# Performance work log

Hardware: AMD Instinct MI355X
Metric: run time of the kernel (lower is better)

Reference implementation:

```python
import jax, jax.numpy as jnp
import numpy as np
from jax import lax

DIM = 1152
HEADS = 16
HEAD_DIM = 72  # HEADS*HEAD_DIM == DIM
HID = 4608     # int(DIM*4.0)
B = 2
N = 4096
EPS_RMS = 1e-6
EPS_LA = 1e-15


def setup_inputs() -> dict:
    key = jax.random.key(0)
    ks = jax.random.split(key, 12)
    w = lambda k, shape: (jax.random.normal(k, shape, jnp.float32) * 0.02)
    z = lambda n: jnp.zeros((n,), jnp.float32)
    return {
        "hidden_states": jax.random.normal(ks[0], (B, N, DIM), jnp.float32),
        "temb": jax.random.normal(ks[1], (B, 6 * DIM), jnp.float32),
        "scale_shift_table": jax.random.normal(ks[2], (6, DIM), jnp.float32) / np.float32(np.sqrt(DIM)),
        "Wq": w(ks[3], (DIM, DIM)), "bq": z(DIM),
        "Wk": w(ks[4], (DIM, DIM)), "bk": z(DIM),
        "Wv": w(ks[5], (DIM, DIM)), "bv": z(DIM),
        "Wo": w(ks[6], (DIM, DIM)), "bo": z(DIM),
        "W_inv": w(ks[7], (2 * HID, DIM)), "b_inv": z(2 * HID),   # 1x1 conv dim -> 2*hid
        "W_dw": w(ks[8], (2 * HID, 3)), "b_dw": z(2 * HID),       # depthwise k=3
        "W_pt": w(ks[9], (DIM, HID)),                              # 1x1 conv hid -> dim, no bias
    }


def _rms(x):
    # RMSNorm, elementwise_affine=False, eps=1e-6
    return x * lax.rsqrt(jnp.mean(x * x, axis=-1, keepdims=True) + EPS_RMS)


def reference(hidden_states, temb, scale_shift_table, Wq, bq, Wk, bk, Wv, bv, Wo, bo,
              W_inv, b_inv, W_dw, b_dw, W_pt):
    Bn, Nn, D = hidden_states.shape
    # adaLN-single modulation
    mods = scale_shift_table[None] + temb.reshape(Bn, 6, D)  # (B,6,D)
    shift_msa, scale_msa, gate_msa, shift_mlp, scale_mlp, gate_mlp = (
        mods[:, i][:, None, :] for i in range(6))  # each (B,1,D)

    x = _rms(hidden_states) * (1.0 + scale_msa) + shift_msa

    # --- Lite linear attention (ReLU kernel, denominator via padded-ones value) ---
    q = jax.nn.relu(x @ Wq.T + bq).reshape(Bn, Nn, HEADS, HEAD_DIM).transpose(0, 2, 1, 3)  # bhnd
    k = jax.nn.relu(x @ Wk.T + bk).reshape(Bn, Nn, HEADS, HEAD_DIM).transpose(0, 2, 1, 3)
    v = (x @ Wv.T + bv).reshape(Bn, Nn, HEADS, HEAD_DIM).transpose(0, 2, 1, 3)
    v = jnp.pad(v, ((0, 0), (0, 0), (0, 0), (0, 1)), constant_values=1.0)  # (B,h,N,d+1)
    kv = jnp.einsum('bhnd,bhne->bhde', k, v)        # (B,h,d,d+1)
    out = jnp.einsum('bhnd,bhde->bhne', q, kv)      # (B,h,N,d+1)
    out = out[..., :-1] / (out[..., -1:] + EPS_LA)  # numerator / denominator
    out = out.transpose(0, 2, 1, 3).reshape(Bn, Nn, D)
    attn_out = out @ Wo.T + bo

    hidden_states = gate_msa * attn_out + hidden_states

    # --- GLUMBConv FFN ---
    y = _rms(hidden_states) * (1.0 + scale_mlp) + shift_mlp
    y = jax.nn.silu(y @ W_inv.T + b_inv)            # inverted 1x1 conv + SiLU, (B,N,2*HID)
    yc = y.transpose(0, 2, 1)                        # (B,2*HID,N)
    yc = lax.conv_general_dilated(
        yc, W_dw[:, None, :], window_strides=(1,), padding=[(1, 1)],
        feature_group_count=2 * HID,
        dimension_numbers=('NCH', 'OIH', 'NCH')) + b_dw[None, :, None]
    xg, gate = jnp.split(yc, 2, axis=1)
    y = (xg * jax.nn.silu(gate)).transpose(0, 2, 1)  # (B,N,HID)
    ff = y @ W_pt.T                                   # point conv, no bias

    return hidden_states + gate_mlp * ff
```

## Files before the change

kernel.cpp:

```cpp
#include <hip/hip_runtime.h>
#include <hip/hip_bf16.h>

typedef __hip_bfloat16 bf16;
typedef short short8 __attribute__((ext_vector_type(8)));
typedef float floatx4 __attribute__((ext_vector_type(4)));
typedef int int4v __attribute__((ext_vector_type(4)));

#define DIMC 1152
#define NTOK 8192
#define NSEQ 4096
#define HD 72
#define HDP 73
#define HIDC 4608
#define HID2 9216
#define QKVN 3456
#define KVH (HD * HDP)
#define PZ ((size_t)2048 * DIMC)
#define PZB ((size_t)4096 * DIMC)

#define DP 96
#define KVNT 128
#define KV_NITER 2
#define KV_CHUNKS 16

__device__ __forceinline__ float b2f(bf16 x) { return __bfloat162float(x); }
__device__ __forceinline__ bf16 f2b(float x) { return __float2bfloat16(x); }
__device__ __forceinline__ void st(float* p, float v) { *p = v; }
__device__ __forceinline__ void st(bf16* p, float v)  { *p = f2b(v); }
__device__ __forceinline__ float tf(float x) { return x; }
__device__ __forceinline__ float tf(bf16 x)  { return __bfloat162float(x); }
__device__ __forceinline__ float s2f(short s) {
    unsigned int u = ((unsigned int)(unsigned short)s) << 16;
    return __uint_as_float(u);
}
__device__ __forceinline__ short f2s(float f) {
    bf16 h = f2b(f);
    return *reinterpret_cast<short*>(&h);
}

__device__ __forceinline__ void gload_lds16(const bf16* g, short* l) {
    __builtin_amdgcn_global_load_lds(
        (const __attribute__((address_space(1))) void*)g,
        (__attribute__((address_space(3))) void*)l, 16, 0, 0);
}

__global__ void cvt_all_kernel(const float* __restrict__ s0, const float* __restrict__ s1,
                               const float* __restrict__ s2, const float* __restrict__ s3,
                               const float* __restrict__ s4, const float* __restrict__ s5,
                               bf16* __restrict__ dst) {
    int i = blockIdx.x * 256 + threadIdx.x;
    if (i >= 5308416) return;
    const float* src; int base;
    if (i < 1327104) {
        if (i < 331776)      { src = s0; base = 0; }
        else if (i < 663552) { src = s1; base = 331776; }
        else if (i < 995328) { src = s2; base = 663552; }
        else                 { src = s3; base = 995328; }
    } else if (i < 3981312)  { src = s4; base = 1327104; }
    else                     { src = s5; base = 3981312; }
    floatx4 v = ((const floatx4*)src)[i - base];
    bf16* o = dst + (size_t)i * 4;
    o[0] = f2b(v[0]); o[1] = f2b(v[1]); o[2] = f2b(v[2]); o[3] = f2b(v[3]);
}

__global__ void bias3_kernel(const float* __restrict__ a, const float* __restrict__ b,
                             const float* __restrict__ c, float* __restrict__ o) {
    int i = blockIdx.x * 256 + threadIdx.x;
    if (i < DIMC) { o[i] = a[i]; o[i + DIMC] = b[i]; o[i + 2 * DIMC] = c[i]; }
}

__global__ void mods_kernel(const float* __restrict__ sst, const float* __restrict__ temb,
                            float* __restrict__ mods) {
    int i = blockIdx.x * 256 + threadIdx.x;
    if (i < 2 * 6 * DIMC) {
        int j = i % (6 * DIMC);
        mods[i] = sst[j] + temb[i];
    }
}

template<typename T>
__global__ void rmsmod_kernel(const T* __restrict__ h, const float* __restrict__ mods,
                              int shift_idx, int scale_idx, bf16* __restrict__ xout) {
    int token = blockIdx.x;
    int b = token >> 12;
    int tid = threadIdx.x;
    int wave = tid >> 6, lane = tid & 63;
    const T* hp = h + (size_t)token * DIMC;

    float v[8];
    float s = 0.f;
    if (tid < 144) {
        if constexpr (sizeof(T) == 4) {
            floatx4 a = *(const floatx4*)((const float*)hp + tid * 8);
            floatx4 c = *(const floatx4*)((const float*)hp + tid * 8 + 4);
            v[0]=a[0]; v[1]=a[1]; v[2]=a[2]; v[3]=a[3];
            v[4]=c[0]; v[5]=c[1]; v[6]=c[2]; v[7]=c[3];
        } else {
            short8 a = *(const short8*)((const short*)hp + tid * 8);
            #pragma unroll
            for (int j = 0; j < 8; j++) v[j] = s2f(a[j]);
        }
        #pragma unroll
        for (int j = 0; j < 8; j++) s += v[j] * v[j];
    }
    #pragma unroll
    for (int off = 32; off > 0; off >>= 1) s += __shfl_down(s, off);
    __shared__ float wsum[4];
    if (lane == 0) wsum[wave] = s;
    __syncthreads();
    float tot = wsum[0] + wsum[1] + wsum[2] + wsum[3];
    float r = rsqrtf(tot / (float)DIMC + 1e-6f);

    if (tid < 144) {
        const float* sh = mods + (size_t)(b * 6 + shift_idx) * DIMC + tid * 8;
        const float* sc = mods + (size_t)(b * 6 + scale_idx) * DIMC + tid * 8;
        floatx4 sh0 = *(const floatx4*)sh, sh1 = *(const floatx4*)(sh + 4);
        floatx4 sc0 = *(const floatx4*)sc, sc1 = *(const floatx4*)(sc + 4);
        short8 o;
        o[0] = f2s(v[0] * r * (1.f + sc0[0]) + sh0[0]);
        o[1] = f2s(v[1] * r * (1.f + sc0[1]) + sh0[1]);
        o[2] = f2s(v[2] * r * (1.f + sc0[2]) + sh0[2]);
        o[3] = f2s(v[3] * r * (1.f + sc0[3]) + sh0[3]);
        o[4] = f2s(v[4] * r * (1.f + sc1[0]) + sh1[0]);
        o[5] = f2s(v[5] * r * (1.f + sc1[1]) + sh1[1]);
        o[6] = f2s(v[6] * r * (1.f + sc1[2]) + sh1[2]);
        o[7] = f2s(v[7] * r * (1.f + sc1[3]) + sh1[3]);
        *(short8*)((short*)xout + (size_t)token * DIMC + tid * 8) = o;
    }
}

template<int MODE, typename OT>
__global__ __launch_bounds__(256, 2)
void gemm_kernel(const bf16* __restrict__ A, const bf16* __restrict__ W,
                 const float* __restrict__ bias, const float* __restrict__ mods,
                 int gate_idx, int m_off, const float* __restrict__ resid,
                 OT* __restrict__ out, int N, int Kfull, int Klen,
                 size_t zstride, int bm_lo, int bm_hi) {
    const int bm = blockIdx.x;
    if (bm < bm_lo || bm >= bm_hi) return;
    const int koff = blockIdx.z * Klen;
    __shared__ __align__(16) short As[128 * 64];
    __shared__ __align__(16) short Bs[128 * 64];
    const int tid = threadIdx.x;
    const int wave = tid >> 6;
    const int lane = tid & 63;
    const int quad = lane >> 4;
    const int l16 = lane & 15;
    const int wm = (wave & 1) * 64;
    const int wn = (wave >> 1) * 64;
    const int bn = blockIdx.y;

    floatx4 acc[4][4];
    #pragma unroll
    for (int i = 0; i < 4; i++)
        #pragma unroll
        for (int j = 0; j < 4; j++)
            #pragma unroll
            for (int r = 0; r < 4; r++) acc[i][j][r] = 0.0f;

    const int lrow8 = lane >> 3;
    const int scol = ((lane & 7) ^ lrow8) * 8;
    const bf16* gA = A + (size_t)(bm * 128 + wave * 8 + lrow8) * Kfull + koff + scol;
    const bf16* gB = W + (size_t)(bn * 128 + wave * 8 + lrow8) * Kfull + koff + scol;
    short* lA = &As[wave * 512];
    short* lB = &Bs[wave * 512];
    const size_t rstep = (size_t)32 * Kfull;

    for (int k0 = 0; k0 < Klen; k0 += 64) {
        __syncthreads();
        #pragma unroll
        for (int j = 0; j < 4; j++) gload_lds16(gA + j * rstep + k0, lA + j * 2048);
        #pragma unroll
        for (int j = 0; j < 4; j++) gload_lds16(gB + j * rstep + k0, lB + j * 2048);
        __syncthreads();
        short8 af[2][4], bfr[2][4];
        #pragma unroll
        for (int i = 0; i < 4; i++) {
            const int ra = wm + i * 16 + l16;
            const int rb = wn + i * 16 + l16;
            #pragma unroll
            for (int kk = 0; kk < 2; kk++) {
                af[kk][i]  = *(const short8*)&As[ra * 64 + (((kk * 4 + quad) ^ (ra & 7)) * 8)];
                bfr[kk][i] = *(const short8*)&Bs[rb * 64 + (((kk * 4 + quad) ^ (rb & 7)) * 8)];
            }
        }
        #pragma unroll
        for (int kk = 0; kk < 2; kk++)
            #pragma unroll
            for (int i = 0; i < 4; i++)
                #pragma unroll
                for (int j = 0; j < 4; j++)
                    acc[i][j] = __builtin_amdgcn_mfma_f32_16x16x32_bf16(af[kk][i], bfr[kk][j], acc[i][j], 0, 0, 0);
    }

    #pragma unroll
    for (int i = 0; i < 4; i++) {
        #pragma unroll
        for (int j = 0; j < 4; j++) {
            const int col = bn * 128 + wn + j * 16 + l16;
            #pragma unroll
            for (int r = 0; r < 4; r++) {
                const int m = bm * 128 + wm + i * 16 + quad * 4 + r;
                float v = acc[i][j][r];
                float o;
                if (MODE == 0) {
                    o = v + bias[col];
                    if (col < 2 * DIMC) o = fmaxf(o, 0.f);
                } else if (MODE == 2) {
                    int b = (m + m_off) >> 12;
                    o = mods[(size_t)(b * 6 + gate_idx) * DIMC + col] * (v + bias[col])
                        + resid[(size_t)m * DIMC + col];
                } else if (MODE == 3) {
                    float sv = v + bias[col];
                    o = sv / (1.f + __expf(-sv));
                } else {
                    o = v;
                }
                st(&out[zstride * blockIdx.z + (size_t)m * N + col], o);
            }
        }
    }
}

__global__ void reduce_kernel(const float* __restrict__ part, const bf16* __restrict__ trunk,
                              const float* __restrict__ mods, int b, int r0, size_t pstride,
                              float* __restrict__ out) {
    int i = blockIdx.x * 256 + threadIdx.x;
    int col = i % DIMC;
    float s = part[i] + part[i + pstride] + part[i + 2 * pstride] + part[i + 3 * pstride];
    size_t gidx = ((size_t)b * NSEQ + r0) * DIMC + i;
    float gate = mods[(size_t)(b * 6 + 5) * DIMC + col];
    out[gidx] = b2f(trunk[gidx]) + gate * s;
}

__device__ __forceinline__ int kvaddr(int row, int n) {
    return row * KVNT + ((((n >> 3) ^ (row & 7))) << 3) + (n & 7);
}

__global__ __launch_bounds__(256, 3)
void attn_kv_kernel(const bf16* __restrict__ qkv, float* __restrict__ part) {
    const int chunk = blockIdx.x;
    const int h = blockIdx.y;
    const int b = blockIdx.z;
    __shared__ __align__(16) short kl[DP * KVNT];
    __shared__ __align__(16) short vl[DP * KVNT];
    const int tid = threadIdx.x;
    const int wave = tid >> 6, lane = tid & 63;
    const int quad = lane >> 4, l16 = lane & 15;
    const int wd = (wave & 1) * 48;
    const int we = (wave >> 1) * 48;

    for (int i = tid; i < 24 * KVNT; i += 256) {
        kl[72 * KVNT + i] = 0;
        vl[72 * KVNT + i] = (i < KVNT) ? (short)0x3F80 : (short)0;
    }

    floatx4 acc[3][3];
    #pragma unroll
    for (int i = 0; i < 3; i++)
        #pragma unroll
        for (int j = 0; j < 3; j++)
            #pragma unroll
            for (int r = 0; r < 4; r++) acc[i][j][r] = 0.0f;

    const size_t tok0 = (size_t)b * NSEQ + (size_t)chunk * (KVNT * KV_NITER);
    for (int it = 0; it < KV_NITER; ++it) {
        __syncthreads();
        const short* rb = (const short*)qkv + (tok0 + (size_t)it * KVNT) * QKVN + h * HD;
        #pragma unroll
        for (int p = 0; p < 5; ++p) {
            int idx = p * 256 + tid;
            int o = idx >> 7, n = idx & 127;
            if (o < 9) {
                const short* g = rb + (size_t)n * QKVN + o * 8;
                short8 kk = *(const short8*)(g + DIMC);
                short8 vv = *(const short8*)(g + 2 * DIMC);
                #pragma unroll
                for (int j = 0; j < 8; ++j) {
                    kl[kvaddr(o * 8 + j, n)] = kk[j];
                    vl[kvaddr(o * 8 + j, n)] = vv[j];
                }
            }
        }
        __syncthreads();
        #pragma unroll
        for (int ks = 0; ks < 4; ++ks) {
            const int nb = ks * 32 + quad * 8;
            short8 af[3], bfv[3];
            #pragma unroll
            for (int i = 0; i < 3; ++i) {
                const int ra = wd + i * 16 + l16;
                const int rbn = we + i * 16 + l16;
                af[i]  = *(const short8*)&kl[ra * KVNT + ((((nb >> 3) ^ (ra & 7))) << 3)];
                bfv[i] = *(const short8*)&vl[rbn * KVNT + ((((nb >> 3) ^ (rbn & 7))) << 3)];
            }
            #pragma unroll
            for (int i = 0; i < 3; ++i)
                #pragma unroll
                for (int j = 0; j < 3; ++j)
                    acc[i][j] = __builtin_amdgcn_mfma_f32_16x16x32_bf16(af[i], bfv[j], acc[i][j], 0, 0, 0);
        }
    }

    float* op = part + ((size_t)((b * 16 + h) * KV_CHUNKS + chunk)) * KVH;
    #pragma unroll
    for (int i = 0; i < 3; ++i) {
        const int dbase = wd + i * 16 + quad * 4;
        #pragma unroll
        for (int j = 0; j < 3; ++j) {
            const int e = we + j * 16 + l16;
            if (e < HDP) {
                #pragma unroll
                for (int r = 0; r < 4; ++r) {
                    const int d = dbase + r;
                    if (d < HD) op[d * HDP + e] = acc[i][j][r];
                }
            }
        }
    }
}

__global__ void kvred_kernel(const float* __restrict__ part, float* __restrict__ kvout) {
    int i = blockIdx.x * 256 + threadIdx.x;
    if (i >= 32 * KVH) return;
    int bh = i / KVH, cell = i - bh * KVH;
    const float* p = part + ((size_t)bh * KV_CHUNKS) * KVH + cell;
    float s = 0.f;
    #pragma unroll
    for (int c = 0; c < KV_CHUNKS; ++c) s += p[(size_t)c * KVH];
    kvout[i] = s;
}

__global__ __launch_bounds__(256, 2)
void attn_out_kernel(const bf16* __restrict__ qkv, const float* __restrict__ kv,
                     bf16* __restrict__ outa) {
    const int chunk = blockIdx.x;
    const int h = blockIdx.y;
    const int b = blockIdx.z;
    __shared__ __align__(16) short ql[128 * 128];
    __shared__ __align__(16) short kvt[80 * 128];
    const int tid = threadIdx.x;
    const int wave = tid >> 6, lane = tid & 63;
    const int quad = lane >> 4, l16 = lane & 15;
    const int wm = wave * 32;

    const short* qbase = (const short*)qkv + ((size_t)(b * NSEQ) + (size_t)chunk * 128) * QKVN + h * HD;
    #pragma unroll
    for (int t = 0; t < 8; ++t) {
        int idx = t * 256 + tid;
        int o = idx >> 7, n = idx & 127;
        short8 vv = {0, 0, 0, 0, 0, 0, 0, 0};
        if (o < 9) vv = *(const short8*)(qbase + (size_t)n * QKVN + o * 8);
        *(short8*)&ql[n * 128 + ((o ^ (n & 7)) << 3)] = vv;
    }
    const float* kp = kv + (size_t)(b * 16 + h) * KVH;
    #pragma unroll
    for (int t = 0; t < 5; ++t) {
        int idx = t * 256 + tid;
        int o = idx / 80, e = idx - (idx / 80) * 80;
        short8 vv = {0, 0, 0, 0, 0, 0, 0, 0};
        if (e < HDP && o < 9) {
            #pragma unroll
            for (int j = 0; j < 8; ++j) {
                int d = o * 8 + j;
                if (d < HD) vv[j] = f2s(kp[(size_t)d * HDP + e]);
            }
        }
        *(short8*)&kvt[e * 128 + ((o ^ (e & 7)) << 3)] = vv;
    }
    __syncthreads();

    floatx4 acc[2][5];
    #pragma unroll
    for (int i = 0; i < 2; ++i)
        #pragma unroll
        for (int j = 0; j < 5; ++j)
            #pragma unroll
            for (int r = 0; r < 4; ++r) acc[i][j][r] = 0.0f;

    #pragma unroll
    for (int kk = 0; kk < 3; ++kk) {
        const int s = kk * 4 + quad;
        short8 af[2];
        #pragma unroll
        for (int i = 0; i < 2; ++i) {
            const int ra = wm + i * 16 + l16;
            af[i] = *(const short8*)&ql[ra * 128 + ((s ^ (ra & 7)) << 3)];
        }
        #pragma unroll
        for (int j = 0; j < 5; ++j) {
            const int rb = j * 16 + l16;
            short8 bfv = *(const short8*)&kvt[rb * 128 + ((s ^ (rb & 7)) << 3)];
            #pragma unroll
            for (int i = 0; i < 2; ++i)
                acc[i][j] = __builtin_amdgcn_mfma_f32_16x16x32_bf16(af[i], bfv, acc[i][j], 0, 0, 0);
        }
    }

    #pragma unroll
    for (int i = 0; i < 2; ++i) {
        #pragma unroll
        for (int r = 0; r < 4; ++r) {
            float den = __shfl(acc[i][4][r], (lane & 48) | 8);
            float inv = 1.0f / (den + 1e-15f);
            const int m = wm + i * 16 + quad * 4 + r;
            bf16* op = outa + ((size_t)(b * NSEQ) + (size_t)chunk * 128 + m) * DIMC + h * HD;
            #pragma unroll
            for (int j = 0; j < 5; ++j) {
                const int e = j * 16 + l16;
                if (e < HD) op[e] = f2b(acc[i][j][r] * inv);
            }
        }
    }
}

__global__ __launch_bounds__(576)
void dwglu_kernel(const bf16* __restrict__ ybuf, const float* __restrict__ wdw,
                  const float* __restrict__ bdw, int r0, int rowoff, bf16* __restrict__ outg) {
    int nl = blockIdx.x;
    int g = r0 + nl;
    int c = threadIdx.x * 8;
    int cg = c + HIDC;
    size_t base = (size_t)(nl + rowoff) * HID2;
    const short* yb = (const short*)ybuf;
    short8 zr = {0, 0, 0, 0, 0, 0, 0, 0};
    bool hm = (g > 0), hp = (g < NSEQ - 1);
    short8 xm = hm ? *(const short8*)(yb + base - HID2 + c)  : zr;
    short8 x0 =      *(const short8*)(yb + base + c);
    short8 xp = hp ? *(const short8*)(yb + base + HID2 + c)  : zr;
    short8 gm = hm ? *(const short8*)(yb + base - HID2 + cg) : zr;
    short8 g0 =      *(const short8*)(yb + base + cg);
    short8 gp = hp ? *(const short8*)(yb + base + HID2 + cg) : zr;
    float wx[24], wg[24], bxv[8], bgv[8];
    #pragma unroll
    for (int t = 0; t < 6; t++) {
        *(floatx4*)&wx[t * 4] = *(const floatx4*)(wdw + (size_t)c * 3 + t * 4);
        *(floatx4*)&wg[t * 4] = *(const floatx4*)(wdw + (size_t)cg * 3 + t * 4);
    }
    *(floatx4*)&bxv[0] = *(const floatx4*)(bdw + c);
    *(floatx4*)&bxv[4] = *(const floatx4*)(bdw + c + 4);
    *(floatx4*)&bgv[0] = *(const floatx4*)(bdw + cg);
    *(floatx4*)&bgv[4] = *(const floatx4*)(bdw + cg + 4);
    short8 o;
    #pragma unroll
    for (int j = 0; j < 8; j++) {
        float a  = s2f(xm[j]) * wx[j * 3] + s2f(x0[j]) * wx[j * 3 + 1]
                 + s2f(xp[j]) * wx[j * 3 + 2] + bxv[j];
        float gg = s2f(gm[j]) * wg[j * 3] + s2f(g0[j]) * wg[j * 3 + 1]
                 + s2f(gp[j]) * wg[j * 3 + 2] + bgv[j];
        float sg = gg / (1.f + __expf(-gg));
        o[j] = f2s(a * sg);
    }
    *(short8*)((short*)outg + (size_t)nl * HIDC + c) = o;
}

extern "C" void kernel_launch(void* const* d_in, const int* in_sizes, int n_in,
                              void* d_out, int out_size, void* d_ws, size_t ws_size,
                              hipStream_t stream) {
    const float* h_in = (const float*)d_in[0];
    const float* temb = (const float*)d_in[1];
    const float* sst  = (const float*)d_in[2];
    const float* Wq = (const float*)d_in[3];   const float* bq_ = (const float*)d_in[4];
    const float* Wk = (const float*)d_in[5];   const float* bk_ = (const float*)d_in[6];
    const float* Wv = (const float*)d_in[7];   const float* bv_ = (const float*)d_in[8];
    const float* Wo = (const float*)d_in[9];   const float* bo_ = (const float*)d_in[10];
    const float* Winv = (const float*)d_in[11]; const float* binv = (const float*)d_in[12];
    const float* Wdw  = (const float*)d_in[13]; const float* bdw  = (const float*)d_in[14];
    const float* Wpt  = (const float*)d_in[15];
    float* out = (float*)d_out;

    const int WSMALL = DIMC * DIMC;
    const int WINVN  = HID2 * DIMC;
    const int WPTN   = DIMC * HIDC;

    char* basep = (char*)d_ws;
    size_t off = 0;
    auto alloc = [&](size_t bytes) -> char* {
        char* p = basep + off;
        off += (bytes + 255) & ~(size_t)255;
        return p;
    };
    float* modsb = (float*)alloc((size_t)2 * 6 * DIMC * 4);
    float* kvb   = (float*)alloc((size_t)32 * KVH * 4);
    float* kvpart = (float*)alloc((size_t)32 * KV_CHUNKS * KVH * 4);
    float* bqkv  = (float*)alloc((size_t)QKVN * 4);
    bf16* wqkv = (bf16*)alloc((size_t)3 * WSMALL * 2);
    bf16* wob  = (bf16*)alloc((size_t)WSMALL * 2);
    bf16* wib  = (bf16*)alloc((size_t)WINVN * 2);
    bf16* wpb  = (bf16*)alloc((size_t)WPTN * 2);
    bf16* bx    = (bf16*)alloc((size_t)NTOK * DIMC * 2);
    bf16* trunk = (bf16*)alloc((size_t)NTOK * DIMC * 2);

    const size_t BGLU_B = (size_t)NSEQ * HIDC * 2;
    const size_t BBIG_B = (size_t)NSEQ * HID2 * 2;
    bool bigws = (ws_size >= off + BGLU_B + BBIG_B + 1024);
    char* R = alloc(bigws ? (BGLU_B + BBIG_B) : (size_t)61341696);
    bf16* qkvb = (bf16*)R;

    cvt_all_kernel<<<20736, 256, 0, stream>>>(Wq, Wk, Wv, Wo, Winv, Wpt, wqkv);
    bias3_kernel<<<5, 256, 0, stream>>>(bq_, bk_, bv_, bqkv);
    mods_kernel<<<54, 256, 0, stream>>>(sst, temb, modsb);
    rmsmod_kernel<float><<<NTOK, 256, 0, stream>>>(h_in, modsb, 0, 1, bx);

    gemm_kernel<0, bf16><<<dim3(NTOK / 128, QKVN / 128), 256, 0, stream>>>(
        bx, wqkv, bqkv, nullptr, 0, 0, nullptr, qkvb, QKVN, DIMC, DIMC, 0, 0, 1 << 30);

    attn_kv_kernel<<<dim3(KV_CHUNKS, 16, 2), 256, 0, stream>>>(qkvb, kvpart);
    kvred_kernel<<<(32 * KVH + 255) / 256, 256, 0, stream>>>(kvpart, kvb);
    attn_out_kernel<<<dim3(32, 16, 2), 256, 0, stream>>>(qkvb, kvb, bx);
    gemm_kernel<2, bf16><<<dim3(NTOK / 128, DIMC / 128), 256, 0, stream>>>(
        bx, wob, bo_, modsb, 2, 0, h_in, trunk, DIMC, DIMC, DIMC, 0, 0, 1 << 30);
    rmsmod_kernel<bf16><<<NTOK, 256, 0, stream>>>(trunk, modsb, 3, 4, bx);

    if (bigws) {
        bf16*  bglu = (bf16*)R;
        bf16*  bbig = (bf16*)(R + BGLU_B);
        float* partials = (float*)(R + BGLU_B);
        for (int b = 0; b < 2; ++b) {
            const bf16* Ainv = bx + (size_t)b * NSEQ * DIMC;
            gemm_kernel<3, bf16><<<dim3(NSEQ / 128, HID2 / 128), 256, 0, stream>>>(
                Ainv, wib, binv, nullptr, 0, 0, nullptr, bbig, HID2, DIMC, DIMC, 0, 0, 1 << 30);
            dwglu_kernel<<<dim3(NSEQ), 576, 0, stream>>>(bbig, Wdw, bdw, 0, 0, bglu);
            gemm_kernel<5, float><<<dim3(32, DIMC / 128, 4), 256, 0, stream>>>(
                bglu, wpb, nullptr, nullptr, 0, 0, nullptr, partials, DIMC, HIDC, HIDC / 4,
                PZB, 0, 1 << 30);
            reduce_kernel<<<(int)(PZB / 256), 256, 0, stream>>>(partials, trunk, modsb, b, 0,
                                                                PZB, out);
        }
    } else {
        bf16*  bglu_c   = (bf16*)R;
        bf16*  bbig_c   = (bf16*)(R + (size_t)18874368);
        float* partials = (float*)(R + (size_t)18874368);
        for (int b = 0; b < 2; ++b) {
            for (int c = 0; c < 2; ++c) {
                int r0 = c * 2048;
                int lo = (c == 0) ? 1 : 0;
                int hi = (c == 0) ? 18 : 17;
                const bf16* Ainv = bx + ((size_t)(b * NSEQ + r0)) * DIMC - (size_t)128 * DIMC;
                gemm_kernel<3, bf16><<<dim3(18, HID2 / 128), 256, 0, stream>>>(
                    Ainv, wib, binv, nullptr, 0, 0, nullptr, bbig_c, HID2, DIMC, DIMC, 0, lo, hi);
                dwglu_kernel<<<dim3(2048), 576, 0, stream>>>(bbig_c, Wdw, bdw, r0, 128, bglu_c);
                gemm_kernel<5, float><<<dim3(16, DIMC / 128, 4), 256, 0, stream>>>(
                    bglu_c, wpb, nullptr, nullptr, 0, 0, nullptr, partials, DIMC, HIDC, HIDC / 4,
                    PZ, 0, 1 << 30);
                reduce_kernel<<<(int)(PZ / 256), 256, 0, stream>>>(partials, trunk, modsb, b, r0,
                                                                   PZ, out);
            }
        }
    }
}
```

Before: 812.9 us.

## Vectorize split-K reduce, halve split-K, fuse prep kernels, remap dwglu blocks

Merges the bias-concat and modulation kernels into one launch. Vectorizes the split-K reduction to float4 loads and stores and templates it on the partition count. In the big-workspace path the point-conv GEMM now uses 2 K-splits instead of 4, which halves the partial traffic but gives that GEMM half as many blocks. The dwglu block index is also permuted across 8 groups, likely to spread row accesses differently across the chip.

```diff
diff --git a/kernel.cpp b/kernel.cpp
--- a/kernel.cpp
+++ b/kernel.cpp
@@ -3,6 +3,7 @@
 
 typedef __hip_bfloat16 bf16;
 typedef short short8 __attribute__((ext_vector_type(8)));
+typedef short short4v __attribute__((ext_vector_type(4)));
 typedef float floatx4 __attribute__((ext_vector_type(4)));
 typedef int int4v __attribute__((ext_vector_type(4)));
 
@@ -63,18 +64,16 @@
     o[0] = f2b(v[0]); o[1] = f2b(v[1]); o[2] = f2b(v[2]); o[3] = f2b(v[3]);
 }
 
-__global__ void bias3_kernel(const float* __restrict__ a, const float* __restrict__ b,
-                             const float* __restrict__ c, float* __restrict__ o) {
-    int i = blockIdx.x * 256 + threadIdx.x;
-    if (i < DIMC) { o[i] = a[i]; o[i + DIMC] = b[i]; o[i + 2 * DIMC] = c[i]; }
-}
-
-__global__ void mods_kernel(const float* __restrict__ sst, const float* __restrict__ temb,
-                            float* __restrict__ mods) {
+__global__ void prep_kernel(const float* __restrict__ sst, const float* __restrict__ temb,
+                            float* __restrict__ mods, const float* __restrict__ ba,
+                            const float* __restrict__ bb, const float* __restrict__ bc,
+                            float* __restrict__ bq) {
     int i = blockIdx.x * 256 + threadIdx.x;
     if (i < 2 * 6 * DIMC) {
-        int j = i % (6 * DIMC);
-        mods[i] = sst[j] + temb[i];
+        mods[i] = sst[i % (6 * DIMC)] + temb[i];
+    } else if (i < 2 * 6 * DIMC + DIMC) {
+        int j = i - 2 * 6 * DIMC;
+        bq[j] = ba[j]; bq[j + DIMC] = bb[j]; bq[j + 2 * DIMC] = bc[j];
     }
 }
 
@@ -222,15 +221,25 @@
     }
 }
 
+template<int NP>
 __global__ void reduce_kernel(const float* __restrict__ part, const bf16* __restrict__ trunk,
                               const float* __restrict__ mods, int b, int r0, size_t pstride,
                               float* __restrict__ out) {
-    int i = blockIdx.x * 256 + threadIdx.x;
-    int col = i % DIMC;
-    float s = part[i] + part[i + pstride] + part[i + 2 * pstride] + part[i + 3 * pstride];
-    size_t gidx = ((size_t)b * NSEQ + r0) * DIMC + i;
-    float gate = mods[(size_t)(b * 6 + 5) * DIMC + col];
-    out[gidx] = b2f(trunk[gidx]) + gate * s;
+    int i4 = (blockIdx.x * 256 + threadIdx.x) * 4;
+    int col = i4 % DIMC;
+    floatx4 s = *(const floatx4*)(part + i4);
+    #pragma unroll
+    for (int p = 1; p < NP; ++p) {
+        floatx4 t = *(const floatx4*)(part + (size_t)p * pstride + i4);
+        s[0] += t[0]; s[1] += t[1]; s[2] += t[2]; s[3] += t[3];
+    }
+    size_t gidx = ((size_t)b * NSEQ + r0) * DIMC + i4;
+    short4v tr = *(const short4v*)((const short*)trunk + gidx);
+    floatx4 g = *(const floatx4*)(mods + (size_t)(b * 6 + 5) * DIMC + col);
+    floatx4 o;
+    #pragma unroll
+    for (int j = 0; j < 4; ++j) o[j] = s2f(tr[j]) + g[j] * s[j];
+    *(floatx4*)(out + gidx) = o;
 }
 
 __device__ __forceinline__ int kvaddr(int row, int n) {
@@ -417,7 +426,9 @@
 __global__ __launch_bounds__(576)
 void dwglu_kernel(const bf16* __restrict__ ybuf, const float* __restrict__ wdw,
                   const float* __restrict__ bdw, int r0, int rowoff, bf16* __restrict__ outg) {
-    int nl = blockIdx.x;
+    int bid = blockIdx.x;
+    int nper = gridDim.x >> 3;
+    int nl = (bid & 7) * nper + (bid >> 3);
     int g = r0 + nl;
     int c = threadIdx.x * 8;
     int cg = c + HIDC;
@@ -498,8 +509,7 @@
     bf16* qkvb = (bf16*)R;
 
     cvt_all_kernel<<<20736, 256, 0, stream>>>(Wq, Wk, Wv, Wo, Winv, Wpt, wqkv);
-    bias3_kernel<<<5, 256, 0, stream>>>(bq_, bk_, bv_, bqkv);
-    mods_kernel<<<54, 256, 0, stream>>>(sst, temb, modsb);
+    prep_kernel<<<59, 256, 0, stream>>>(sst, temb, modsb, bq_, bk_, bv_, bqkv);
     rmsmod_kernel<float><<<NTOK, 256, 0, stream>>>(h_in, modsb, 0, 1, bx);
 
     gemm_kernel<0, bf16><<<dim3(NTOK / 128, QKVN / 128), 256, 0, stream>>>(
@@ -521,11 +531,11 @@
             gemm_kernel<3, bf16><<<dim3(NSEQ / 128, HID2 / 128), 256, 0, stream>>>(
                 Ainv, wib, binv, nullptr, 0, 0, nullptr, bbig, HID2, DIMC, DIMC, 0, 0, 1 << 30);
             dwglu_kernel<<<dim3(NSEQ), 576, 0, stream>>>(bbig, Wdw, bdw, 0, 0, bglu);
-            gemm_kernel<5, float><<<dim3(32, DIMC / 128, 4), 256, 0, stream>>>(
-                bglu, wpb, nullptr, nullptr, 0, 0, nullptr, partials, DIMC, HIDC, HIDC / 4,
+            gemm_kernel<5, float><<<dim3(32, DIMC / 128, 2), 256, 0, stream>>>(
+                bglu, wpb, nullptr, nullptr, 0, 0, nullptr, partials, DIMC, HIDC, HIDC / 2,
                 PZB, 0, 1 << 30);
-            reduce_kernel<<<(int)(PZB / 256), 256, 0, stream>>>(partials, trunk, modsb, b, 0,
-                                                                PZB, out);
+            reduce_kernel<2><<<(int)(PZB / 1024), 256, 0, stream>>>(partials, trunk, modsb, b, 0,
+                                                                    PZB, out);
         }
     } else {
         bf16*  bglu_c   = (bf16*)R;
@@ -543,9 +553,9 @@
                 gemm_kernel<5, float><<<dim3(16, DIMC / 128, 4), 256, 0, stream>>>(
                     bglu_c, wpb, nullptr, nullptr, 0, 0, nullptr, partials, DIMC, HIDC, HIDC / 4,
                     PZ, 0, 1 << 30);
-                reduce_kernel<<<(int)(PZ / 256), 256, 0, stream>>>(partials, trunk, modsb, b, r0,
-                                                                   PZ, out);
-            }
-        }
-    }
-}
+                reduce_kernel<4><<<(int)(PZ / 1024), 256, 0, stream>>>(partials, trunk, modsb, b,
+                                                                       r0, PZ, out);
+            }
+        }
+    }
+}
```

After: 778.0 us. 1.04x faster.
